# Optimization experiments

Measured on AMD Instinct MI355X. Metric: run time of the kernel, lower is better.

## Reference

```python
import jax, jax.numpy as jnp
import numpy as np

TN = 2.0  # near plane
TF = 6.0  # far plane
FAR_DELTA = 1e10  # sentinel last-bin width, as in the torch code


def setup_inputs() -> dict:
    key = jax.random.key(0)
    k1, k2, k3, k4, k5, k6 = jax.random.split(key, 6)
    N = 200_000
    ray_o = jax.random.normal(k1, (N, 3), dtype=jnp.float32) * 0.1
    ray_d = jax.random.normal(k2, (N, 3), dtype=jnp.float32)
    ray_d = ray_d / jnp.linalg.norm(ray_d, axis=-1, keepdims=True)
    w_d = jax.random.normal(k3, (3,), dtype=jnp.float32) * 0.5
    b_d = jax.random.normal(k4, (1,), dtype=jnp.float32) * 0.1
    w_c = jax.random.normal(k5, (3, 3), dtype=jnp.float32) * 0.5
    b_c = jax.random.normal(k6, (3,), dtype=jnp.float32) * 0.1
    return {"ray_o": ray_o, "ray_d": ray_d, "w_d": w_d, "b_d": b_d,
            "w_c": w_c, "b_c": b_c, "n_bins": 128}


def _integrate(p, w_d, b_d, w_c, b_c):
    # Surrogate BaseObject.integrate: density [N,B], color [N,B,3]
    d = jax.nn.softplus(jnp.einsum('nbk,k->nb', p, w_d) + b_d[0])
    c = jax.nn.sigmoid(jnp.einsum('nbk,kj->nbj', p, w_c) + b_c)
    return c, d


def reference(ray_o, ray_d, w_d, b_d, w_c, b_c, n_bins):
    t = jnp.linspace(TN, TF, n_bins, dtype=ray_o.dtype)            # [B]
    # sample points along each ray: [N, B, 3]
    p = ray_o[:, None, :] + t[None, :, None] * ray_d[:, None, :]
    c, d = _integrate(p, w_d, b_d, w_c, b_c)
    delta = jnp.concatenate([t[1:] - t[:-1],
                             jnp.asarray([FAR_DELTA], dtype=t.dtype)])  # [B]
    T = jnp.exp(-delta[None, :] * d)                               # [N, B]
    alpha = 1.0 - T
    acc_t = jnp.cumprod(T, axis=1)
    # exclusive transmittance: shift right, prepend ones
    acc_t = jnp.concatenate([jnp.ones((acc_t.shape[0], 1), dtype=T.dtype),
                             acc_t[:, :-1]], axis=1)
    weight = acc_t * alpha                                         # [N, B]
    return jnp.einsum('nb,nbj->nj', weight, c)                     # [N, 3]
```

## Files before the change

### kernel.cpp

```cpp
#include <hip/hip_runtime.h>
#include <hip/hip_bf16.h>

#define NBINS 128
#define TN_ 2.0f
#define TF_ 6.0f
#define FAR_DELTA_ 1e10f
#define LOG2E_ 1.44269504088896340736f
#define BINS_PER_LANE 64
#define U_SMALL 9.5367431640625e-7f

__device__ __forceinline__ float rcp_fast(float x)  { return __builtin_amdgcn_rcpf(x); }
__device__ __forceinline__ float exp2_fast(float x) { return __builtin_amdgcn_exp2f(x); }
__device__ __forceinline__ float log2_fast(float x) { return __builtin_amdgcn_logf(x); }

__global__ __launch_bounds__(256) void volrender_kernel(
    const float* __restrict__ ray_o,
    const float* __restrict__ ray_d,
    const float* __restrict__ w_d,
    const float* __restrict__ b_d,
    const float* __restrict__ w_c,
    const float* __restrict__ b_c,
    float* __restrict__ out,
    int N)
{
    const int tid = blockIdx.x * 256 + threadIdx.x;
    const int n   = tid >> 1;
    const int sub = tid & 1;
    if (n >= N) return;

    const float ox = ray_o[n * 3 + 0];
    const float oy = ray_o[n * 3 + 1];
    const float oz = ray_o[n * 3 + 2];
    const float dx = ray_d[n * 3 + 0];
    const float dy = ray_d[n * 3 + 1];
    const float dz = ray_d[n * 3 + 2];

    const float wd0 = w_d[0], wd1 = w_d[1], wd2 = w_d[2];
    const float bd  = b_d[0];
    float wcm[9];
#pragma unroll
    for (int k = 0; k < 9; ++k) wcm[k] = w_c[k];
    const float bc0 = b_c[0], bc1 = b_c[1], bc2 = b_c[2];

    const float a_o = fmaf(oz, wd2, fmaf(oy, wd1, ox * wd0)) + bd;
    const float a_d = fmaf(dz, wd2, fmaf(dy, wd1, dx * wd0));
    const float aLo = a_o * LOG2E_;
    const float aLd = a_d * LOG2E_;
    float co0 = fmaf(oz, wcm[6], fmaf(oy, wcm[3], ox * wcm[0])) + bc0;
    float co1 = fmaf(oz, wcm[7], fmaf(oy, wcm[4], ox * wcm[1])) + bc1;
    float co2 = fmaf(oz, wcm[8], fmaf(oy, wcm[5], ox * wcm[2])) + bc2;
    float cd0 = fmaf(dz, wcm[6], fmaf(dy, wcm[3], dx * wcm[0]));
    float cd1 = fmaf(dz, wcm[7], fmaf(dy, wcm[4], dx * wcm[1]));
    float cd2 = fmaf(dz, wcm[8], fmaf(dy, wcm[5], dx * wcm[2]));
    const float nco0 = -co0 * LOG2E_, ncd0 = -cd0 * LOG2E_;
    const float nco1 = -co1 * LOG2E_, ncd1 = -cd1 * LOG2E_;
    const float nco2 = -co2 * LOG2E_, ncd2 = -cd2 * LOG2E_;

    const float dt   = (TF_ - TN_) / (float)(NBINS - 1);
    const float ndt  = -dt;
    const float ndLast = (sub == 1) ? -FAR_DELTA_ : ndt;
    const float t0   = fmaf((float)(sub * BINS_PER_LANE), dt, TN_);
    const float dt8  = 8.0f * dt;

    float um = exp2_fast(fmaf(fmaf(3.5f, dt, t0), aLd, aLo));
    const float Ku8 = exp2_fast(aLd * dt8);

    float x0 = exp2_fast(fmaf(t0, ncd0, nco0));
    float x1 = exp2_fast(fmaf(t0, ncd1, nco1));
    float x2 = exp2_fast(fmaf(t0, ncd2, nco2));
    const float K0 = exp2_fast(ncd0 * dt8);
    const float K1 = exp2_fast(ncd1 * dt8);
    const float K2 = exp2_fast(ncd2 * dt8);

    float c0, c1, c2;
    {
        const float A = 1.f + x0, B = 1.f + x1, C = 1.f + x2;
        const float BC = B * C;
        const float r  = rcp_fast(A * BC);
        c0 = BC * r;
        c1 = (A * C) * r;
        c2 = (A * B) * r;
    }

    float Pprev = 1.0f;
    float o0 = 0.f, o1 = 0.f, o2 = 0.f;

#pragma unroll
    for (int s = 0; s < (BINS_PER_LANE / 8) - 1; ++s) {
        x0 *= K0; x1 *= K1; x2 *= K2;
        float cE0, cE1, cE2;
        {
            const float A = 1.f + x0, B = 1.f + x1, C = 1.f + x2;
            const float BC = B * C;
            const float r  = rcp_fast(A * BC);
            cE0 = BC * r;
            cE1 = (A * C) * r;
            cE2 = (A * B) * r;
        }
        const float dc0 = (cE0 - c0) * 0.125f;
        const float dc1 = (cE1 - c1) * 0.125f;
        const float dc2 = (cE2 - c2) * 0.125f;

        const float f    = log2_fast(1.0f + um);
        um *= Ku8;
        const float rho  = exp2_fast(ndt * f);
        const float rho2 = rho * rho, rho4 = rho2 * rho2, rho8 = rho4 * rho4;
        const float P8   = Pprev * rho8;
        const float S0   = Pprev - P8;
        const float S8   = (1.f + rho) * (1.f + rho2) * (1.f + rho4);
        const float S1   = fmaf(-7.f, P8, Pprev * (S8 - 1.f));

        o0 = fmaf(c0, S0, fmaf(dc0, S1, o0));
        o1 = fmaf(c1, S0, fmaf(dc1, S1, o1));
        o2 = fmaf(c2, S0, fmaf(dc2, S1, o2));
        c0 = cE0; c1 = cE1; c2 = cE2;
        Pprev = P8;
    }

    {
        x0 *= K0; x1 *= K1; x2 *= K2;
        float cE0, cE1, cE2;
        {
            const float A = 1.f + x0, B = 1.f + x1, C = 1.f + x2;
            const float BC = B * C;
            const float r  = rcp_fast(A * BC);
            cE0 = BC * r;
            cE1 = (A * C) * r;
            cE2 = (A * B) * r;
        }
        const float dc0 = (cE0 - c0) * 0.125f;
        const float dc1 = (cE1 - c1) * 0.125f;
        const float dc2 = (cE2 - c2) * 0.125f;

        const float f    = log2_fast(1.0f + um);
        const float rho  = exp2_fast(ndt * f);
        const float rho2 = rho * rho;
        const float rho3 = rho2 * rho;
        const float rho4 = rho2 * rho2;
        const float P6   = Pprev * (rho4 * rho3);

        const float t63 = fmaf(63.f, dt, t0);
        const float u63 = exp2_fast(fmaf(t63, aLd, aLo));
        float v7 = log2_fast(1.f + u63);
        v7 = (u63 < U_SMALL) ? u63 * LOG2E_ : v7;
        const float T7 = exp2_fast(ndLast * v7);
        const float P7 = P6 * T7;

        const float inner = rho * fmaf(rho, 1.f + rho, 1.f);
        const float G     = inner * (1.f + rho3);
        const float S0    = Pprev - P7;
        const float S1    = fmaf(Pprev, G, P6 * fmaf(-7.f, T7, 1.f));

        o0 = fmaf(c0, S0, fmaf(dc0, S1, o0));
        o1 = fmaf(c1, S0, fmaf(dc1, S1, o1));
        o2 = fmaf(c2, S0, fmaf(dc2, S1, o2));
        Pprev = P7;
    }

    {
        const float q0 = __shfl_down(o0, 1, 2);
        const float q1 = __shfl_down(o1, 1, 2);
        const float q2 = __shfl_down(o2, 1, 2);
        o0 = fmaf(Pprev, q0, o0);
        o1 = fmaf(Pprev, q1, o1);
        o2 = fmaf(Pprev, q2, o2);
    }

    if (sub == 0) {
        out[n * 3 + 0] = o0;
        out[n * 3 + 1] = o1;
        out[n * 3 + 2] = o2;
    }
}

extern "C" void kernel_launch(void* const* d_in, const int* in_sizes, int n_in,
                              void* d_out, int out_size, void* d_ws, size_t ws_size,
                              hipStream_t stream) {
    const float* ray_o = (const float*)d_in[0];
    const float* ray_d = (const float*)d_in[1];
    const float* w_d   = (const float*)d_in[2];
    const float* b_d   = (const float*)d_in[3];
    const float* w_c   = (const float*)d_in[4];
    const float* b_c   = (const float*)d_in[5];

    float* out = (float*)d_out;
    const int N = in_sizes[0] / 3;

    const int threads = N * 2;
    const int block = 256;
    const int grid  = (threads + block - 1) / block;
    volrender_kernel<<<grid, block, 0, stream>>>(ray_o, ray_d, w_d, b_d, w_c, b_c, out, N);
}
```

Baseline: 11.65 us.

## Share density evaluation across 16 bins and batch paired color reciprocals

The main loop now handles two 8-bin color segments per iteration. It evaluates the softplus density once per 16 bins instead of once per 8, and reuses the same rho powers for both halves. The two sigmoid color evaluations share one reciprocal through a cross-multiplied denominator. This cuts the log2, exp2 and rcp work per ray. In exchange, density is held constant over wider intervals, which makes the transmittance approximation coarser and increases error.

```diff
diff --git a/kernel.cpp b/kernel.cpp
--- a/kernel.cpp
+++ b/kernel.cpp
@@ -62,8 +62,8 @@
     const float t0   = fmaf((float)(sub * BINS_PER_LANE), dt, TN_);
     const float dt8  = 8.0f * dt;
 
-    float um = exp2_fast(fmaf(fmaf(3.5f, dt, t0), aLd, aLo));
-    const float Ku8 = exp2_fast(aLd * dt8);
+    float um = exp2_fast(fmaf(fmaf(7.5f, dt, t0), aLd, aLo));
+    const float Ku16 = exp2_fast(aLd * (16.0f * dt));
 
     float x0 = exp2_fast(fmaf(t0, ncd0, nco0));
     float x1 = exp2_fast(fmaf(t0, ncd1, nco1));
@@ -86,75 +86,69 @@
     float o0 = 0.f, o1 = 0.f, o2 = 0.f;
 
 #pragma unroll
-    for (int s = 0; s < (BINS_PER_LANE / 8) - 1; ++s) {
-        x0 *= K0; x1 *= K1; x2 *= K2;
-        float cE0, cE1, cE2;
-        {
-            const float A = 1.f + x0, B = 1.f + x1, C = 1.f + x2;
-            const float BC = B * C;
-            const float r  = rcp_fast(A * BC);
-            cE0 = BC * r;
-            cE1 = (A * C) * r;
-            cE2 = (A * B) * r;
-        }
-        const float dc0 = (cE0 - c0) * 0.125f;
-        const float dc1 = (cE1 - c1) * 0.125f;
-        const float dc2 = (cE2 - c2) * 0.125f;
+    for (int S = 0; S < 4; ++S) {
+        const float xa0 = x0 * K0, xb0 = xa0 * K0;
+        const float xa1 = x1 * K1, xb1 = xa1 * K1;
+        const float xa2 = x2 * K2, xb2 = xa2 * K2;
+        x0 = xb0; x1 = xb1; x2 = xb2;
+        const float Aa = 1.f + xa0, Ba = 1.f + xa1, Ca = 1.f + xa2;
+        const float Ab = 1.f + xb0, Bb = 1.f + xb1, Cb = 1.f + xb2;
+        const float BCa = Ba * Ca, ACa = Aa * Ca, ABa = Aa * Ba;
+        const float BCb = Bb * Cb, ACb = Ab * Cb, ABb = Ab * Bb;
+        const float Da = Aa * BCa, Db = Ab * BCb;
+        const float r  = rcp_fast(Da * Db);
+        const float rA = r * Db, rB = r * Da;
+        const float cA0 = BCa * rA, cA1 = ACa * rA, cA2 = ABa * rA;
+        const float cB0 = BCb * rB, cB1 = ACb * rB, cB2 = ABb * rB;
 
         const float f    = log2_fast(1.0f + um);
-        um *= Ku8;
+        um *= Ku16;
         const float rho  = exp2_fast(ndt * f);
         const float rho2 = rho * rho, rho4 = rho2 * rho2, rho8 = rho4 * rho4;
-        const float P8   = Pprev * rho8;
-        const float S0   = Pprev - P8;
-        const float S8   = (1.f + rho) * (1.f + rho2) * (1.f + rho4);
-        const float S1   = fmaf(-7.f, P8, Pprev * (S8 - 1.f));
+        const float S8m1 = (1.f + rho) * (1.f + rho2) * (1.f + rho4) - 1.f;
 
-        o0 = fmaf(c0, S0, fmaf(dc0, S1, o0));
-        o1 = fmaf(c1, S0, fmaf(dc1, S1, o1));
-        o2 = fmaf(c2, S0, fmaf(dc2, S1, o2));
-        c0 = cE0; c1 = cE1; c2 = cE2;
-        Pprev = P8;
-    }
+        {
+            const float P8 = Pprev * rho8;
+            const float S0 = Pprev - P8;
+            const float s1 = 0.125f * fmaf(-7.f, P8, Pprev * S8m1);
+            const float dc0 = cA0 - c0, dc1 = cA1 - c1, dc2 = cA2 - c2;
+            o0 = fmaf(c0, S0, fmaf(dc0, s1, o0));
+            o1 = fmaf(c1, S0, fmaf(dc1, s1, o1));
+            o2 = fmaf(c2, S0, fmaf(dc2, s1, o2));
+            Pprev = P8;
+        }
+        if (S < 3) {
+            const float P8 = Pprev * rho8;
+            const float S0 = Pprev - P8;
+            const float s1 = 0.125f * fmaf(-7.f, P8, Pprev * S8m1);
+            const float dc0 = cB0 - cA0, dc1 = cB1 - cA1, dc2 = cB2 - cA2;
+            o0 = fmaf(cA0, S0, fmaf(dc0, s1, o0));
+            o1 = fmaf(cA1, S0, fmaf(dc1, s1, o1));
+            o2 = fmaf(cA2, S0, fmaf(dc2, s1, o2));
+            Pprev = P8;
+        } else {
+            const float rho3 = rho2 * rho;
+            const float rho7 = rho4 * rho3;
+            const float P6   = Pprev * rho7;
 
-    {
-        x0 *= K0; x1 *= K1; x2 *= K2;
-        float cE0, cE1, cE2;
-        {
-            const float A = 1.f + x0, B = 1.f + x1, C = 1.f + x2;
-            const float BC = B * C;
-            const float r  = rcp_fast(A * BC);
-            cE0 = BC * r;
-            cE1 = (A * C) * r;
-            cE2 = (A * B) * r;
+            const float t63 = fmaf(63.f, dt, t0);
+            const float u63 = exp2_fast(fmaf(t63, aLd, aLo));
+            float v7 = log2_fast(1.f + u63);
+            v7 = (u63 < U_SMALL) ? u63 * LOG2E_ : v7;
+            const float T7 = exp2_fast(ndLast * v7);
+            const float P7 = P6 * T7;
+
+            const float inner = rho * fmaf(rho, 1.f + rho, 1.f);
+            const float G     = inner * (1.f + rho3);
+            const float S0    = Pprev - P7;
+            const float s1    = 0.125f * fmaf(Pprev, G, P6 * fmaf(-7.f, T7, 1.f));
+            const float dc0 = cB0 - cA0, dc1 = cB1 - cA1, dc2 = cB2 - cA2;
+            o0 = fmaf(cA0, S0, fmaf(dc0, s1, o0));
+            o1 = fmaf(cA1, S0, fmaf(dc1, s1, o1));
+            o2 = fmaf(cA2, S0, fmaf(dc2, s1, o2));
+            Pprev = P7;
         }
-        const float dc0 = (cE0 - c0) * 0.125f;
-        const float dc1 = (cE1 - c1) * 0.125f;
-        const float dc2 = (cE2 - c2) * 0.125f;
-
-        const float f    = log2_fast(1.0f + um);
-        const float rho  = exp2_fast(ndt * f);
-        const float rho2 = rho * rho;
-        const float rho3 = rho2 * rho;
-        const float rho4 = rho2 * rho2;
-        const float P6   = Pprev * (rho4 * rho3);
-
-        const float t63 = fmaf(63.f, dt, t0);
-        const float u63 = exp2_fast(fmaf(t63, aLd, aLo));
-        float v7 = log2_fast(1.f + u63);
-        v7 = (u63 < U_SMALL) ? u63 * LOG2E_ : v7;
-        const float T7 = exp2_fast(ndLast * v7);
-        const float P7 = P6 * T7;
-
-        const float inner = rho * fmaf(rho, 1.f + rho, 1.f);
-        const float G     = inner * (1.f + rho3);
-        const float S0    = Pprev - P7;
-        const float S1    = fmaf(Pprev, G, P6 * fmaf(-7.f, T7, 1.f));
-
-        o0 = fmaf(c0, S0, fmaf(dc0, S1, o0));
-        o1 = fmaf(c1, S0, fmaf(dc1, S1, o1));
-        o2 = fmaf(c2, S0, fmaf(dc2, S1, o2));
-        Pprev = P7;
+        c0 = cB0; c1 = cB1; c2 = cB2;
     }
 
     {
```

Measured after the change: 10.63 us, median of 2. 1.1x faster.
